# Optimization experiments

Measured on AMD Instinct MI355X. Metric: run time of the kernel, lower is better.

Reference implementation:

```python
import jax, jax.numpy as jnp
import numpy as np

B, IN, C, H, E = 8192, 768, 64, 64, 16  # batch, input_dim, n_concepts, hidden_dim, embedding_dim


def setup_inputs() -> dict:
    key = jax.random.key(0)
    ks = jax.random.split(key, 10)

    def w(k, shape, fan_in):
        return jax.random.normal(k, shape, jnp.float32) / np.float32(np.sqrt(fan_in))

    inp = {"x": jax.random.normal(ks[0], (B, IN), jnp.float32)}
    i = 1
    for pre, din, dout in (("pos", IN, E), ("neg", IN, E), ("cp", 2 * E, 1)):
        inp[pre + "_W1"] = w(ks[i], (C, din, H), din)
        inp[pre + "_b1"] = jnp.zeros((C, H), jnp.float32)
        inp[pre + "_W2"] = w(ks[i + 1], (C, H, H), H)
        inp[pre + "_b2"] = jnp.zeros((C, H), jnp.float32)
        inp[pre + "_W3"] = w(ks[i + 2], (C, H, dout), H)
        inp[pre + "_b3"] = jnp.zeros((C, dout), jnp.float32)
        i += 3
    return inp


def _bank(x, W1, b1, W2, b2, W3, b3):
    # x: [B, IN]; per-concept MLP batched over C via einsum -> [B, C, E]
    h = jax.nn.relu(jnp.einsum('bi,cih->bch', x, W1) + b1)
    h = jax.nn.relu(jnp.einsum('bch,cho->bco', h, W2) + b2)
    return jnp.einsum('bch,che->bce', h, W3) + b3


def reference(x, pos_W1, pos_b1, pos_W2, pos_b2, pos_W3, pos_b3,
              neg_W1, neg_b1, neg_W2, neg_b2, neg_W3, neg_b3,
              cp_W1, cp_b1, cp_W2, cp_b2, cp_W3, cp_b3):
    pos = _bank(x, pos_W1, pos_b1, pos_W2, pos_b2, pos_W3, pos_b3)  # [B,C,E]
    neg = _bank(x, neg_W1, neg_b1, neg_W2, neg_b2, neg_W3, neg_b3)  # [B,C,E]
    # torch cat([pos, neg], dim=1) on [B,E,C], then x[:,:,i] -> per-concept [B, 2E]
    xc = jnp.concatenate([pos, neg], axis=-1)  # [B,C,2E]
    h = jax.nn.relu(jnp.einsum('bci,cih->bch', xc, cp_W1) + cp_b1)
    h = jax.nn.relu(jnp.einsum('bch,cho->bco', h, cp_W2) + cp_b2)
    concepts = (jnp.einsum('bch,cho->bco', h, cp_W3) + cp_b3)[..., 0]  # [B,C]
    w = jnp.clip(concepts * 0.5 + 0.5, 0.0, 1.0)[:, :, None]  # gate in [0,1]
    emb = pos * w + neg * (1.0 - w)  # [B,C,E]
    # torch layout is [B,E,C] then .view(B,-1): transpose before flattening
    emb_flat = jnp.transpose(emb, (0, 2, 1)).reshape(x.shape[0], E * C)
    return emb_flat, concepts
```

## Files before the change

### kernel.cpp

```cpp
#include <hip/hip_runtime.h>
#include <hip/hip_bf16.h>


#define B_   8192
#define IN_  768
#define C_   64
#define H_   64
#define E_   16
#define BM_  128

typedef __bf16 bf16x8 __attribute__((ext_vector_type(8)));
typedef float  f32x4  __attribute__((ext_vector_type(4)));

__device__ __forceinline__ f32x4 mfma16(bf16x8 a, bf16x8 b, f32x4 c) {
  return __builtin_amdgcn_mfma_f32_16x16x32_bf16(a, b, c, 0, 0, 0);
}

__device__ __forceinline__ bf16x8 cvt8(float4 a, float4 b) {
  bf16x8 r;
  r[0] = (__bf16)a.x; r[1] = (__bf16)a.y; r[2] = (__bf16)a.z; r[3] = (__bf16)a.w;
  r[4] = (__bf16)b.x; r[5] = (__bf16)b.y; r[6] = (__bf16)b.z; r[7] = (__bf16)b.w;
  return r;
}

__device__ __forceinline__ void zero_acc(f32x4 (&acc)[2][4]) {
  const f32x4 z = {0.f, 0.f, 0.f, 0.f};
#pragma unroll
  for (int mt = 0; mt < 2; ++mt)
#pragma unroll
    for (int nt = 0; nt < 4; ++nt) acc[mt][nt] = z;
}

struct __align__(16) SmemT {
  __bf16 xs[BM_ * 72];
  __bf16 wt[128 * 72];
  __bf16 xcb[BM_ * 40];
  float  conc[BM_];
};
static_assert(sizeof(SmemT) == 47616, "layout");
static_assert(sizeof(SmemT) <= 54613, "LDS: need 3 blocks/CU");

__device__ __forceinline__ void epi72(__bf16* __restrict__ hb, f32x4 (&acc)[2][4],
                                      const float* __restrict__ bias,
                                      int wave, int quad, int l16) {
#pragma unroll
  for (int nt = 0; nt < 4; ++nt) {
    const int col = nt * 16 + l16;
    const float bv = bias[col];
#pragma unroll
    for (int mt = 0; mt < 2; ++mt)
#pragma unroll
      for (int r = 0; r < 4; ++r) {
        int row = wave * 32 + mt * 16 + quad * 4 + r;
        hb[row * 72 + col] = (__bf16)fmaxf(acc[mt][nt][r] + bv, 0.f);
      }
  }
}

__device__ __forceinline__ void gemm64(const __bf16* __restrict__ hb,
                                       const __bf16* __restrict__ wt,
                                       f32x4 (&acc)[2][4], int wave, int quad, int l16) {
#pragma unroll
  for (int ks = 0; ks < 2; ++ks) {
    bf16x8 a[2], bb[4];
#pragma unroll
    for (int mt = 0; mt < 2; ++mt)
      a[mt] = *(const bf16x8*)(hb + (wave * 32 + mt * 16 + l16) * 72 + ks * 32 + quad * 8);
#pragma unroll
    for (int nt = 0; nt < 4; ++nt)
      bb[nt] = *(const bf16x8*)(wt + (nt * 16 + l16) * 72 + ks * 32 + quad * 8);
#pragma unroll
    for (int mt = 0; mt < 2; ++mt)
#pragma unroll
      for (int nt = 0; nt < 4; ++nt)
        acc[mt][nt] = mfma16(a[mt], bb[nt], acc[mt][nt]);
  }
}

__device__ __forceinline__ void stage_w64(const __bf16* __restrict__ Wt,
                                          __bf16* __restrict__ wt, int tid) {
#pragma unroll
  for (int it = 0; it < 2; ++it) {
    int q = tid + it * 256;
    int n = q >> 3, i = q & 7;
    *(uint4*)&wt[n * 72 + i * 8] = *(const uint4*)(Wt + n * 64 + i * 8);
  }
}

__device__ __forceinline__ void l3_tile(const __bf16* __restrict__ hb,
                                        const __bf16* __restrict__ wt16,
                                        __bf16* __restrict__ xcb,
                                        const float* __restrict__ b3, int xc_off,
                                        int wave, int quad, int l16) {
  f32x4 acc3[2];
  { const f32x4 z = {0.f, 0.f, 0.f, 0.f}; acc3[0] = z; acc3[1] = z; }
#pragma unroll
  for (int ks = 0; ks < 2; ++ks) {
    bf16x8 bb = *(const bf16x8*)(wt16 + l16 * 72 + ks * 32 + quad * 8);
#pragma unroll
    for (int mt = 0; mt < 2; ++mt) {
      bf16x8 a = *(const bf16x8*)(hb + (wave * 32 + mt * 16 + l16) * 72 + ks * 32 + quad * 8);
      acc3[mt] = mfma16(a, bb, acc3[mt]);
    }
  }
  const float bv = b3[l16];
#pragma unroll
  for (int mt = 0; mt < 2; ++mt)
#pragma unroll
    for (int r = 0; r < 4; ++r) {
      int row = wave * 32 + mt * 16 + quad * 4 + r;
      xcb[row * 40 + xc_off + l16] = (__bf16)(acc3[mt][r] + bv);
    }
}

__global__ __launch_bounds__(256, 3) void cb_fused_t(
    const __bf16* __restrict__ x,
    const __bf16* __restrict__ pW1t, const float* __restrict__ pb1,
    const __bf16* __restrict__ pW2t, const float* __restrict__ pb2,
    const __bf16* __restrict__ pW3t, const float* __restrict__ pb3,
    const __bf16* __restrict__ nW1t, const float* __restrict__ nb1,
    const __bf16* __restrict__ nW2t, const float* __restrict__ nb2,
    const __bf16* __restrict__ nW3t, const float* __restrict__ nb3,
    const __bf16* __restrict__ cW1t, const float* __restrict__ cb1,
    const __bf16* __restrict__ cW2t, const float* __restrict__ cb2,
    const __bf16* __restrict__ cw3,  const float* __restrict__ cb3,
    float* __restrict__ out_emb, float* __restrict__ out_con)
{
  __shared__ SmemT sm;
  const int tid  = threadIdx.x;
  const int wave = tid >> 6, lane = tid & 63;
  const int quad = lane >> 4, l16 = lane & 15;
  const int row0 = blockIdx.x * BM_;
  const int c    = blockIdx.y;
  __bf16* xs = sm.xs;
  __bf16* wt = sm.wt;
  __bf16* hb = sm.xs;

  const __bf16* pg   = pW1t + (size_t)c * 64 * IN_;
  const __bf16* ng   = nW1t + (size_t)c * 64 * IN_;
  const float*  pb1c = pb1 + c * 64;
  const float*  nb1c = nb1 + c * 64;
  const float*  pb2c = pb2 + c * 64;
  const float*  nb2c = nb2 + c * 64;

  f32x4 accP[2][4]; zero_acc(accP);
  f32x4 accN[2][4]; zero_acc(accN);
  const int sr = tid >> 3, si = tid & 7;
  const __bf16* xg = x + (size_t)row0 * IN_;
  for (int kt = 0; kt < IN_ / 64; ++kt) {
    const int ko = kt * 64;
    uint4 xv[4], pv[2], nv[2];
#pragma unroll
    for (int it = 0; it < 4; ++it)
      xv[it] = *(const uint4*)(xg + (size_t)(sr + it * 32) * IN_ + ko + si * 8);
#pragma unroll
    for (int it = 0; it < 2; ++it) {
      pv[it] = *(const uint4*)(pg + (size_t)(sr + it * 32) * IN_ + ko + si * 8);
      nv[it] = *(const uint4*)(ng + (size_t)(sr + it * 32) * IN_ + ko + si * 8);
    }
#pragma unroll
    for (int it = 0; it < 4; ++it)
      *(uint4*)&xs[(sr + it * 32) * 72 + si * 8] = xv[it];
#pragma unroll
    for (int it = 0; it < 2; ++it) {
      *(uint4*)&wt[(sr + it * 32) * 72 + si * 8]        = pv[it];
      *(uint4*)&wt[(64 + sr + it * 32) * 72 + si * 8]   = nv[it];
    }
    __syncthreads();
#pragma unroll
    for (int ks = 0; ks < 2; ++ks) {
      bf16x8 a[2], bp[4], bn[4];
#pragma unroll
      for (int mt = 0; mt < 2; ++mt)
        a[mt] = *(const bf16x8*)&xs[(wave * 32 + mt * 16 + l16) * 72 + ks * 32 + quad * 8];
#pragma unroll
      for (int nt = 0; nt < 4; ++nt) {
        bp[nt] = *(const bf16x8*)&wt[(nt * 16 + l16) * 72 + ks * 32 + quad * 8];
        bn[nt] = *(const bf16x8*)&wt[(64 + nt * 16 + l16) * 72 + ks * 32 + quad * 8];
      }
#pragma unroll
      for (int mt = 0; mt < 2; ++mt)
#pragma unroll
        for (int nt = 0; nt < 4; ++nt) {
          accP[mt][nt] = mfma16(a[mt], bp[nt], accP[mt][nt]);
          accN[mt][nt] = mfma16(a[mt], bn[nt], accN[mt][nt]);
        }
    }
    __syncthreads();
  }

  epi72(hb, accP, pb1c, wave, quad, l16);
  stage_w64(pW2t + (size_t)c * 64 * 64, wt, tid);
  stage_w64(nW2t + (size_t)c * 64 * 64, wt + 64 * 72, tid);
  __syncthreads();

  f32x4 acc2P[2][4]; zero_acc(acc2P);
  gemm64(hb, wt, acc2P, wave, quad, l16);
  __syncthreads();

  epi72(hb, accN, nb1c, wave, quad, l16);
  {
    int n = tid >> 3, i = tid & 7;
    const __bf16* src = (n < 16)
        ? (pW3t + (size_t)c * 16 * 64 + n * 64 + i * 8)
        : (nW3t + (size_t)c * 16 * 64 + (n - 16) * 64 + i * 8);
    *(uint4*)&wt[n * 72 + i * 8] = *(const uint4*)src;
  }
  __syncthreads();

  f32x4 acc2N[2][4]; zero_acc(acc2N);
  gemm64(hb, wt + 64 * 72, acc2N, wave, quad, l16);
  __syncthreads();

  epi72(hb, acc2P, pb2c, wave, quad, l16);
  __syncthreads();
  l3_tile(hb, wt, sm.xcb, pb3 + c * 16, 0, wave, quad, l16);
  __syncthreads();

  epi72(hb, acc2N, nb2c, wave, quad, l16);
  __syncthreads();
  l3_tile(hb, wt + 16 * 72, sm.xcb, nb3 + c * 16, 16, wave, quad, l16);
  __syncthreads();

  {
    int n = tid >> 2, i = tid & 3;
    *(uint4*)&wt[n * 72 + i * 8] = *(const uint4*)(cW1t + ((size_t)c * 64 + n) * 32 + i * 8);
  }
  __syncthreads();
  f32x4 acc1[2][4]; zero_acc(acc1);
  {
    bf16x8 a[2], bb[4];
#pragma unroll
    for (int mt = 0; mt < 2; ++mt)
      a[mt] = *(const bf16x8*)&sm.xcb[(wave * 32 + mt * 16 + l16) * 40 + quad * 8];
#pragma unroll
    for (int nt = 0; nt < 4; ++nt)
      bb[nt] = *(const bf16x8*)&wt[(nt * 16 + l16) * 72 + quad * 8];
#pragma unroll
    for (int mt = 0; mt < 2; ++mt)
#pragma unroll
      for (int nt = 0; nt < 4; ++nt)
        acc1[mt][nt] = mfma16(a[mt], bb[nt], acc1[mt][nt]);
  }
  __syncthreads();
  epi72(hb, acc1, cb1 + c * 64, wave, quad, l16);
  stage_w64(cW2t + (size_t)c * 64 * 64, wt, tid);
  __syncthreads();

  f32x4 acc2[2][4]; zero_acc(acc2);
  gemm64(hb, wt, acc2, wave, quad, l16);
  __syncthreads();
  epi72(hb, acc2, cb2 + c * 64, wave, quad, l16);
  if (tid < 8) *(uint4*)&wt[tid * 8] = *(const uint4*)(cw3 + (size_t)c * 64 + tid * 8);
  __syncthreads();

  f32x4 acc3[2];
  { const f32x4 z = {0.f, 0.f, 0.f, 0.f}; acc3[0] = z; acc3[1] = z; }
#pragma unroll
  for (int ks = 0; ks < 2; ++ks) {
    bf16x8 bb = {};
    if (l16 == 0) bb = *(const bf16x8*)&wt[ks * 32 + quad * 8];
#pragma unroll
    for (int mt = 0; mt < 2; ++mt) {
      bf16x8 a = *(const bf16x8*)&hb[(wave * 32 + mt * 16 + l16) * 72 + ks * 32 + quad * 8];
      acc3[mt] = mfma16(a, bb, acc3[mt]);
    }
  }
  if (l16 == 0) {
    float bv = cb3[c];
#pragma unroll
    for (int mt = 0; mt < 2; ++mt)
#pragma unroll
      for (int r = 0; r < 4; ++r)
        sm.conc[wave * 32 + mt * 16 + quad * 4 + r] = acc3[mt][r] + bv;
  }
  __syncthreads();

  for (int ii = tid; ii < BM_ * E_; ii += 256) {
    int row = ii >> 4, e = ii & 15;
    float cv = sm.conc[row];
    float w  = fminf(fmaxf(cv * 0.5f + 0.5f, 0.f), 1.f);
    float pv2 = (float)sm.xcb[row * 40 + e];
    float nv2 = (float)sm.xcb[row * 40 + 16 + e];
    out_emb[(size_t)(row0 + row) * (E_ * C_) + e * C_ + c] = pv2 * w + nv2 * (1.f - w);
  }
  if (tid < 128) out_con[(size_t)(row0 + tid) * C_ + c] = sm.conc[tid];
}

#define TSEG 5
#define PSEG 5
struct PrepArgs {
  const float* tsrc[TSEG];
  __bf16*      tdst[TSEG];
  int tstart[TSEG + 1];
  int ktiles[TSEG];
  const float* psrc[PSEG];
  __bf16*      pdst[PSEG];
  int pstart[PSEG + 1];
  int pchunks[PSEG];
  int kdiv8[PSEG];
  int N[PSEG];
  int tblocks;
};

__global__ __launch_bounds__(256) void prep_all(PrepArgs a) {
  const int tid = threadIdx.x;
  const int b = blockIdx.x;
  __shared__ __bf16 lt[64 * 72];
  if (b < a.tblocks) {
    int s = 0;
    while (s < TSEG - 1 && b >= a.tstart[s + 1]) ++s;
    const int idx = b - a.tstart[s];
    const int kt = idx % a.ktiles[s];
    const int c  = idx / a.ktiles[s];
    const int K  = a.ktiles[s] * 64;
    const float* src = a.tsrc[s] + (size_t)c * K * 64 + (size_t)kt * 64 * 64;
    __bf16*      dst = a.tdst[s] + (size_t)c * 64 * K + kt * 64;
    const int r = tid >> 4, c4 = (tid & 15) * 4;
#pragma unroll
    for (int it = 0; it < 4; ++it) {
      int k = r + it * 16;
      float4 v = *(const float4*)(src + (size_t)k * 64 + c4);
      lt[(c4 + 0) * 72 + k] = (__bf16)v.x;
      lt[(c4 + 1) * 72 + k] = (__bf16)v.y;
      lt[(c4 + 2) * 72 + k] = (__bf16)v.z;
      lt[(c4 + 3) * 72 + k] = (__bf16)v.w;
    }
    __syncthreads();
    const int n = tid >> 3, i = tid & 7;
#pragma unroll
    for (int it = 0; it < 2; ++it) {
      int nn = n + it * 32;
      *(uint4*)(dst + (size_t)nn * K + i * 8) = *(const uint4*)&lt[nn * 72 + i * 8];
    }
  } else {
    const int bb = b - a.tblocks;
    int s = 0;
    while (s < PSEG - 1 && bb >= a.pstart[s + 1]) ++s;
    const int lb  = bb - a.pstart[s];
    const int nch = a.pchunks[s];
    const int kc  = a.kdiv8[s];
    const int N   = a.N[s];
#pragma unroll
    for (int j = 0; j < 4; ++j) {
      const int li = (lb * 4 + j) * 256 + tid;
      if (li >= nch) break;
      if (N == 1) {
        const float4* src = (const float4*)a.psrc[s] + (size_t)li * 2;
        float4 v0 = src[0], v1 = src[1];
        *(uint4*)(a.pdst[s] + (size_t)li * 8) = __builtin_bit_cast(uint4, cvt8(v0, v1));
      } else {
        int rn = li / kc;
        int k0 = (li - rn * kc) * 8;
        int cc = rn / N;
        int n  = rn - cc * N;
        const float* src = a.psrc[s] + ((size_t)cc * kc * 8 + k0) * N + n;
        bf16x8 r;
#pragma unroll
        for (int jj = 0; jj < 8; ++jj) r[jj] = (__bf16)src[(size_t)jj * N];
        *(uint4*)(a.pdst[s] + (size_t)rn * kc * 8 + k0) = __builtin_bit_cast(uint4, r);
      }
    }
  }
}

extern "C" void kernel_launch(void* const* d_in, const int* in_sizes, int n_in,
                              void* d_out, int out_size, void* d_ws, size_t ws_size,
                              hipStream_t stream) {
  const float* xf   = (const float*)d_in[0];
  const float* pW1f = (const float*)d_in[1];
  const float* pb1f = (const float*)d_in[2];
  const float* pW2f = (const float*)d_in[3];
  const float* pb2f = (const float*)d_in[4];
  const float* pW3f = (const float*)d_in[5];
  const float* pb3f = (const float*)d_in[6];
  const float* nW1f = (const float*)d_in[7];
  const float* nb1f = (const float*)d_in[8];
  const float* nW2f = (const float*)d_in[9];
  const float* nb2f = (const float*)d_in[10];
  const float* nW3f = (const float*)d_in[11];
  const float* nb3f = (const float*)d_in[12];
  const float* cW1f = (const float*)d_in[13];
  const float* cb1f = (const float*)d_in[14];
  const float* cW2f = (const float*)d_in[15];
  const float* cb2f = (const float*)d_in[16];
  const float* cW3f = (const float*)d_in[17];
  const float* cb3f = (const float*)d_in[18];

  float* out_emb = (float*)d_out;
  float* out_con = out_emb + (size_t)B_ * E_ * C_;

  const int cx   = B_ * IN_;
  const int cW1c = C_ * IN_ * H_;
  const int cW2c = C_ * H_ * H_;
  const int cW3c = C_ * H_ * E_;
  const int ccW1 = C_ * 2 * E_ * H_;
  const int ccW3 = C_ * H_;

  __bf16* w = (__bf16*)d_ws;
  size_t o = 0;
  __bf16* xw   = w + o; o += cx;
  __bf16* pw1t = w + o; o += cW1c;
  __bf16* nw1t = w + o; o += cW1c;
  __bf16* pw2t = w + o; o += cW2c;
  __bf16* nw2t = w + o; o += cW2c;
  __bf16* cw2t = w + o; o += cW2c;
  __bf16* pw3t = w + o; o += cW3c;
  __bf16* nw3t = w + o; o += cW3c;
  __bf16* cw1t = w + o; o += ccW1;
  __bf16* cw3w = w + o; o += ccW3;

  PrepArgs a;
  int tb = 0, pb = 0;
  {
    const float* tsrc[TSEG] = {pW1f, nW1f, pW2f, nW2f, cW2f};
    __bf16*      tdst[TSEG] = {pw1t, nw1t, pw2t, nw2t, cw2t};
    const int    tk[TSEG]   = {12,   12,   1,    1,    1};
    for (int i = 0; i < TSEG; ++i) {
      a.tsrc[i] = tsrc[i]; a.tdst[i] = tdst[i]; a.ktiles[i] = tk[i];
      a.tstart[i] = tb;
      tb += tk[i] * C_;
    }
    a.tstart[TSEG] = tb;
    a.tblocks = tb;

    const float* psrc[PSEG] = {xf, cW3f, pW3f, nW3f, cW1f};
    __bf16*      pdst[PSEG] = {xw, cw3w, pw3t, nw3t, cw1t};
    const int    pKs[PSEG]  = {0,  0,    64,   64,   32};
    const int    pNs[PSEG]  = {1,  1,    16,   16,   64};
    const int    pels[PSEG] = {cx, ccW3, cW3c, cW3c, ccW1};
    for (int i = 0; i < PSEG; ++i) {
      a.psrc[i] = psrc[i]; a.pdst[i] = pdst[i];
      a.pchunks[i] = pels[i] / 8;
      a.kdiv8[i] = (pNs[i] == 1) ? (pels[i] / 8) : (pKs[i] / 8);
      a.N[i] = pNs[i];
      a.pstart[i] = pb;
      pb += (pels[i] / 8 + 1023) / 1024;
    }
    a.pstart[PSEG] = pb;
  }
  prep_all<<<tb + pb, 256, 0, stream>>>(a);

  dim3 grid(B_ / BM_, C_);
  cb_fused_t<<<grid, 256, 0, stream>>>(xw,
      pw1t, pb1f, pw2t, pb2f, pw3t, pb3f,
      nw1t, nb1f, nw2t, nb2f, nw3t, nb3f,
      cw1t, cb1f, cw2t, cb2f, cw3w, cb3f,
      out_emb, out_con);
}
```

Before: 311.9 us.

## Double-buffer layer-1 K loop with direct global-to-LDS loads and XOR swizzle

Rewrites the first-layer K loop so each wave issues global_load_lds transfers straight into a double-buffered LDS region, with an XOR-swizzled 64-wide layout in place of padded rows. The next tile is prefetched while MFMAs run on the current one, and vmcnt waits plus barriers control the handoff. The goal is to hide global latency and skip the register round trip. It doubles LDS use, so occupancy drops from 3 to 2 blocks per CU, and the later stages have to work with the new buffer layout.

```diff
diff --git a/kernel.cpp b/kernel.cpp
--- a/kernel.cpp
+++ b/kernel.cpp
@@ -31,14 +31,22 @@
     for (int nt = 0; nt < 4; ++nt) acc[mt][nt] = z;
 }
 
+__device__ __forceinline__ void gll16(const __bf16* g, __bf16* l) {
+  __builtin_amdgcn_global_load_lds(
+      (const __attribute__((address_space(1))) unsigned int*)g,
+      (__attribute__((address_space(3))) unsigned int*)l, 16, 0, 0);
+}
+
+#define FENCE asm volatile("" ::: "memory")
+
 struct __align__(16) SmemT {
-  __bf16 xs[BM_ * 72];
-  __bf16 wt[128 * 72];
+  __bf16 bufA[256 * 64];
+  __bf16 bufB[256 * 64];
   __bf16 xcb[BM_ * 40];
   float  conc[BM_];
 };
-static_assert(sizeof(SmemT) == 47616, "layout");
-static_assert(sizeof(SmemT) <= 54613, "LDS: need 3 blocks/CU");
+static_assert(sizeof(SmemT) == 76288, "layout");
+static_assert(sizeof(SmemT) <= 81920, "LDS: need 2 blocks/CU");
 
 __device__ __forceinline__ void epi72(__bf16* __restrict__ hb, f32x4 (&acc)[2][4],
                                       const float* __restrict__ bias,
@@ -113,7 +121,33 @@
     }
 }
 
-__global__ __launch_bounds__(256, 3) void cb_fused_t(
+__device__ __forceinline__ void l1_step(const __bf16* __restrict__ cbuf,
+                                        f32x4 (&accP)[2][4], f32x4 (&accN)[2][4],
+                                        int wave, int quad, int l16) {
+  const int sx = l16 & 7;
+#pragma unroll
+  for (int ks = 0; ks < 2; ++ks) {
+    const int pc = (((ks * 4 + quad) ^ sx)) * 8;
+    bf16x8 a[2], bp[4], bn[4];
+#pragma unroll
+    for (int mt = 0; mt < 2; ++mt)
+      a[mt] = *(const bf16x8*)(cbuf + (wave * 32 + mt * 16 + l16) * 64 + pc);
+#pragma unroll
+    for (int nt = 0; nt < 4; ++nt) {
+      bp[nt] = *(const bf16x8*)(cbuf + (128 + nt * 16 + l16) * 64 + pc);
+      bn[nt] = *(const bf16x8*)(cbuf + (192 + nt * 16 + l16) * 64 + pc);
+    }
+#pragma unroll
+    for (int mt = 0; mt < 2; ++mt)
+#pragma unroll
+      for (int nt = 0; nt < 4; ++nt) {
+        accP[mt][nt] = mfma16(a[mt], bp[nt], accP[mt][nt]);
+        accN[mt][nt] = mfma16(a[mt], bn[nt], accN[mt][nt]);
+      }
+  }
+}
+
+__global__ __launch_bounds__(256, 2) void cb_fused_t(
     const __bf16* __restrict__ x,
     const __bf16* __restrict__ pW1t, const float* __restrict__ pb1,
     const __bf16* __restrict__ pW2t, const float* __restrict__ pb2,
@@ -132,9 +166,8 @@
   const int quad = lane >> 4, l16 = lane & 15;
   const int row0 = blockIdx.x * BM_;
   const int c    = blockIdx.y;
-  __bf16* xs = sm.xs;
-  __bf16* wt = sm.wt;
-  __bf16* hb = sm.xs;
+  __bf16* hb = sm.bufA;
+  __bf16* wt = sm.bufB;
 
   const __bf16* pg   = pW1t + (size_t)c * 64 * IN_;
   const __bf16* ng   = nW1t + (size_t)c * 64 * IN_;
@@ -145,49 +178,42 @@
 
   f32x4 accP[2][4]; zero_acc(accP);
   f32x4 accN[2][4]; zero_acc(accN);
-  const int sr = tid >> 3, si = tid & 7;
+
   const __bf16* xg = x + (size_t)row0 * IN_;
-  for (int kt = 0; kt < IN_ / 64; ++kt) {
-    const int ko = kt * 64;
-    uint4 xv[4], pv[2], nv[2];
-#pragma unroll
-    for (int it = 0; it < 4; ++it)
-      xv[it] = *(const uint4*)(xg + (size_t)(sr + it * 32) * IN_ + ko + si * 8);
-#pragma unroll
-    for (int it = 0; it < 2; ++it) {
-      pv[it] = *(const uint4*)(pg + (size_t)(sr + it * 32) * IN_ + ko + si * 8);
-      nv[it] = *(const uint4*)(ng + (size_t)(sr + it * 32) * IN_ + ko + si * 8);
-    }
-#pragma unroll
-    for (int it = 0; it < 4; ++it)
-      *(uint4*)&xs[(sr + it * 32) * 72 + si * 8] = xv[it];
-#pragma unroll
-    for (int it = 0; it < 2; ++it) {
-      *(uint4*)&wt[(sr + it * 32) * 72 + si * 8]        = pv[it];
-      *(uint4*)&wt[(64 + sr + it * 32) * 72 + si * 8]   = nv[it];
-    }
-    __syncthreads();
-#pragma unroll
-    for (int ks = 0; ks < 2; ++ks) {
-      bf16x8 a[2], bp[4], bn[4];
-#pragma unroll
-      for (int mt = 0; mt < 2; ++mt)
-        a[mt] = *(const bf16x8*)&xs[(wave * 32 + mt * 16 + l16) * 72 + ks * 32 + quad * 8];
-#pragma unroll
-      for (int nt = 0; nt < 4; ++nt) {
-        bp[nt] = *(const bf16x8*)&wt[(nt * 16 + l16) * 72 + ks * 32 + quad * 8];
-        bn[nt] = *(const bf16x8*)&wt[(64 + nt * 16 + l16) * 72 + ks * 32 + quad * 8];
-      }
-#pragma unroll
-      for (int mt = 0; mt < 2; ++mt)
-#pragma unroll
-        for (int nt = 0; nt < 4; ++nt) {
-          accP[mt][nt] = mfma16(a[mt], bp[nt], accP[mt][nt]);
-          accN[mt][nt] = mfma16(a[mt], bn[nt], accN[mt][nt]);
-        }
-    }
-    __syncthreads();
-  }
+  const int lrow   = lane >> 3;
+  const int lchunk = (lane & 7) ^ lrow;
+  const __bf16* gsrc = (wave == 0) ? xg
+                     : (wave == 1) ? xg + 64 * IN_
+                     : (wave == 2) ? pg : ng;
+  const __bf16* gl = gsrc + (size_t)lrow * IN_ + lchunk * 8;
+  __bf16* const dA = sm.bufA + wave * 64 * 64;
+  __bf16* const dB = sm.bufB + wave * 64 * 64;
+
+#pragma unroll
+  for (int j = 0; j < 8; ++j)
+    gll16(gl + j * 8 * IN_, dA + j * 8 * 64);
+
+  for (int kt = 0; kt < 11; ++kt) {
+    {
+      const __bf16* gk = gl + (kt + 1) * 64;
+      __bf16* nd = (kt & 1) ? dA : dB;
+#pragma unroll
+      for (int j = 0; j < 8; ++j)
+        gll16(gk + j * 8 * IN_, nd + j * 8 * 64);
+    }
+    asm volatile("s_waitcnt vmcnt(8)" ::: "memory");
+    __builtin_amdgcn_s_barrier();
+    __builtin_amdgcn_sched_barrier(0);
+    FENCE;
+    l1_step((kt & 1) ? sm.bufB : sm.bufA, accP, accN, wave, quad, l16);
+    FENCE;
+    __builtin_amdgcn_s_barrier();
+    __builtin_amdgcn_sched_barrier(0);
+    FENCE;
+  }
+  __syncthreads();
+  l1_step(sm.bufB, accP, accN, wave, quad, l16);
+  __syncthreads();
 
   epi72(hb, accP, pb1c, wave, quad, l16);
   stage_w64(pW2t + (size_t)c * 64 * 64, wt, tid);
```

New measurement: 334.5 us. +7.2%, slower.
